# Optimization experiments

Measured on AMD Instinct MI355X. Metric: run time of the kernel, lower is better.

The kernel has to match this reference:

```python
import jax, jax.numpy as jnp
import numpy as np

N = 1024      # nodes == subgraphs (NGNN: one subgraph per node)
DEG = 8       # average degree
E = N * DEG   # edges
IND = 32      # indim
OUTD = 32     # outdim


def setup_inputs() -> dict:
    key = jax.random.key(0)
    k0, k1, k2, k3, k4 = jax.random.split(key, 5)
    X = jax.random.normal(k0, (N, N, IND), dtype=jnp.float32)
    # binary tuple-support mask (which (i,j) tuples exist in the sparse 2D tensor)
    mask = jax.random.randint(k1, (N, N), 0, 2).astype(jnp.int32)
    # adjacency edge list: A[row, col] = 1 (structure-only sparse adjacency)
    edge_row = jax.random.randint(k2, (E,), 0, N)  # destination j
    edge_col = jax.random.randint(k3, (E,), 0, N)  # source k
    # MLP (single linear layer, PygHO MLP default)
    W = jax.random.normal(k4, (IND, OUTD), dtype=jnp.float32) / np.sqrt(IND).astype(np.float32)
    b = jnp.zeros((OUTD,), dtype=jnp.float32)
    return {"X": X, "mask": mask, "edge_row": edge_row, "edge_col": edge_col, "W": W, "b": b}


def reference(X, mask, edge_row, edge_col, W, b):
    n = X.shape[0]
    m = mask.astype(X.dtype)[..., None]                      # [n, n, 1]
    # tuplewise MLP on existing tuples: tX[i,j] = X[i,j] @ W + b
    tX = (jnp.einsum("ijd,de->ije", X, W) + b) * m           # [n, n, OUTD]
    # message passing within each subgraph i along node dim j:
    # ret[i, j] = sum_{k : A[j,k]=1} tX[i, k]
    msgs = jnp.take(tX, edge_col, axis=1)                    # [n, E, OUTD] gather sources
    msgs = jnp.moveaxis(msgs, 1, 0)                          # [E, n, OUTD]
    agg = jax.ops.segment_sum(msgs, edge_row, num_segments=n)  # [j, i, OUTD]
    ret = jnp.swapaxes(agg, 0, 1) * m                        # restrict to tuple support (tarX = tX)
    return ret
```

## Files before the change

### kernel.cpp

```cpp
#include <hip/hip_runtime.h>


#define NN   1024
#define IND  32
#define OUTD 32
#define EE   8192

typedef __attribute__((ext_vector_type(2))) float f32x2;

__global__ __launch_bounds__(1024) void k_zero(int* __restrict__ p, int n) {
    const int t = blockIdx.x * 1024 + threadIdx.x;
    if (t < n) p[t] = 0;
}

__global__ __launch_bounds__(1024) void k_count(const int* __restrict__ erow,
                                                int* __restrict__ cnt, int n_edges) {
    const int e = blockIdx.x * 1024 + threadIdx.x;
    if (e < n_edges) atomicAdd(&cnt[erow[e]], 1);
}

__global__ __launch_bounds__(1024) void k_scan(const int* __restrict__ cnt,
                                               int* __restrict__ row_ptr,
                                               int* __restrict__ fill) {
    __shared__ int sb[NN];
    const int t = threadIdx.x;
    const int v = cnt[t];
    sb[t] = v;
    __syncthreads();
    #pragma unroll
    for (int off = 1; off < NN; off <<= 1) {
        const int a = (t >= off) ? sb[t - off] : 0;
        __syncthreads();
        sb[t] += a;
        __syncthreads();
    }
    const int excl = sb[t] - v;
    row_ptr[t] = excl;
    fill[t]    = excl;
    if (t == NN - 1) row_ptr[NN] = sb[t];
}

__global__ __launch_bounds__(1024) void k_scatter(const int* __restrict__ erow,
                                                  const int* __restrict__ ecol,
                                                  int* __restrict__ fill,
                                                  int* __restrict__ cols, int n_edges) {
    const int e = blockIdx.x * 1024 + threadIdx.x;
    if (e < n_edges) {
        const int pos = atomicAdd(&fill[erow[e]], 1);
        cols[pos] = ecol[e];
    }
}

__global__ __launch_bounds__(256, 4) void ngnn_main_kernel(
    const float* __restrict__ X, const int* __restrict__ mask,
    const float* __restrict__ W, const float* __restrict__ b,
    const int* __restrict__ row_ptr, const int* __restrict__ cols,
    float* __restrict__ out)
{
    __shared__ float          maskf[NN];
    __shared__ unsigned int   meta[NN];
    __shared__ unsigned short colsl[EE];
    __shared__ unsigned short alist[NN];
    __shared__ int            acount;

    const int t = threadIdx.x;
    const int i = blockIdx.x;

    if (t == 0) acount = 0;
    {
        const int4 m4 = ((const int4*)(mask + (size_t)i * NN))[t];
        maskf[4*t+0] = (float)m4.x; maskf[4*t+1] = (float)m4.y;
        maskf[4*t+2] = (float)m4.z; maskf[4*t+3] = (float)m4.w;
    }
    __syncthreads();

    #pragma unroll
    for (int p = 0; p < 4; ++p) {
        const int j = p * 256 + t;
        if (maskf[j] != 0.f) {
            const int a   = row_ptr[j];
            const int bnd = row_ptr[j + 1];
            int c = 0;
            for (int e = a; e < bnd; ++e) {
                const int k = cols[e] & (NN - 1);
                if (maskf[k] != 0.f) colsl[a + (c++)] = (unsigned short)k;
            }
            meta[j] = (unsigned)a | ((unsigned)c << 16);
            const int pos = atomicAdd(&acount, 1);
            alist[pos] = (unsigned short)j;
        }
    }
    __syncthreads();

    const float4 z = {0.f, 0.f, 0.f, 0.f};
    #pragma unroll
    for (int p = 0; p < 4; ++p) {
        const int j = p * 256 + t;
        if (maskf[j] == 0.f) {
            float4* orow = (float4*)(out + ((size_t)i * NN + j) * OUTD);
            #pragma unroll
            for (int q = 0; q < 8; ++q) orow[q] = z;
        }
    }

    const float4* Xi = (const float4*)(X + (size_t)i * NN * IND);
    const f32x2*  W2 = (const f32x2*)W;
    const f32x2*  b2 = (const f32x2*)b;
    const int na = acount;

    for (int a = t; a < na; a += 256) {
        const int j = (int)alist[a];
        const unsigned md = meta[j];
        const int e0 = (int)(md & 0xffffu);
        const int cn = (int)(md >> 16);

        float4 S4[8];
        #pragma unroll
        for (int s = 0; s < 8; ++s) S4[s] = z;

        for (int q = 0; q < cn; ++q) {
            const int k = (int)colsl[e0 + q];
            const float4* r = Xi + (k << 3);
            #pragma unroll
            for (int s = 0; s < 8; ++s) {
                const float4 v = r[s];
                S4[s].x += v.x; S4[s].y += v.y; S4[s].z += v.z; S4[s].w += v.w;
            }
        }

        const float cf = (float)cn;
        f32x2 o2[16];
        #pragma unroll
        for (int c = 0; c < 16; ++c) o2[c] = b2[c] * cf;
        #pragma unroll
        for (int d = 0; d < IND; ++d) {
            const float sd = ((const float*)S4)[d];
            #pragma unroll
            for (int c = 0; c < 16; ++c) o2[c] += W2[d * 16 + c] * sd;
        }

        float4* orow = (float4*)(out + ((size_t)i * NN + j) * OUTD);
        #pragma unroll
        for (int q2 = 0; q2 < 8; ++q2)
            orow[q2] = make_float4(o2[2*q2].x, o2[2*q2].y, o2[2*q2+1].x, o2[2*q2+1].y);
    }
}

extern "C" void kernel_launch(void* const* d_in, const int* in_sizes, int n_in,
                              void* d_out, int out_size, void* d_ws, size_t ws_size,
                              hipStream_t stream) {
    const float* X    = (const float*)d_in[0];
    const int*   mask = (const int*)d_in[1];
    const int*   erow = (const int*)d_in[2];
    const int*   ecol = (const int*)d_in[3];
    const float* W    = (const float*)d_in[4];
    const float* b    = (const float*)d_in[5];
    float*       out  = (float*)d_out;

    int n_edges = in_sizes[2];
    if (n_edges > EE) n_edges = EE;

    int* cnt     = (int*)d_ws;
    int* row_ptr = cnt + 1024;
    int* fill    = cnt + 2560;
    int* cols    = cnt + 4096;

    const int eb = (n_edges + 1023) / 1024;
    k_zero   <<<1, 1024, 0, stream>>>(cnt, NN);
    k_count  <<<eb, 1024, 0, stream>>>(erow, cnt, n_edges);
    k_scan   <<<1, 1024, 0, stream>>>(cnt, row_ptr, fill);
    k_scatter<<<eb, 1024, 0, stream>>>(erow, ecol, fill, cols, n_edges);

    ngnn_main_kernel<<<NN, 256, 0, stream>>>(X, mask, W, b, row_ptr, cols, out);
}
```

Baseline: 335.9 us.

## Fuse CSR build into one kernel and map output channels to lanes

Combines the four CSR-building kernels into a single-block kernel that counts, scans and scatters in shared memory, which removes launch overhead. The main kernel is restructured so that each wavefront handles two rows, with each lane owning one channel. Lanes gather X coalesced per channel, share partial sums through LDS, and do the 32x32 linear layer from W values held in registers. This replaces the old per-thread, row-serial gather and its big register arrays with coalesced accesses and less register pressure, at the cost of per-row LDS exchange and scalar stores.

```diff
diff --git a/kernel.cpp b/kernel.cpp
--- a/kernel.cpp
+++ b/kernel.cpp
@@ -6,28 +6,29 @@
 #define OUTD 32
 #define EE   8192
 
-typedef __attribute__((ext_vector_type(2))) float f32x2;
+__global__ __launch_bounds__(1024) void k_csr(const int* __restrict__ erow,
+                                              const int* __restrict__ ecol,
+                                              int* __restrict__ row_ptr,
+                                              int* __restrict__ cols,
+                                              int n_edges) {
+    __shared__ int sb[NN];
+    __shared__ int fill[NN];
+    const int t = threadIdx.x;
 
-__global__ __launch_bounds__(1024) void k_zero(int* __restrict__ p, int n) {
-    const int t = blockIdx.x * 1024 + threadIdx.x;
-    if (t < n) p[t] = 0;
-}
-
-__global__ __launch_bounds__(1024) void k_count(const int* __restrict__ erow,
-                                                int* __restrict__ cnt, int n_edges) {
-    const int e = blockIdx.x * 1024 + threadIdx.x;
-    if (e < n_edges) atomicAdd(&cnt[erow[e]], 1);
-}
-
-__global__ __launch_bounds__(1024) void k_scan(const int* __restrict__ cnt,
-                                               int* __restrict__ row_ptr,
-                                               int* __restrict__ fill) {
-    __shared__ int sb[NN];
-    const int t = threadIdx.x;
-    const int v = cnt[t];
-    sb[t] = v;
+    int er[8], ec[8];
+    #pragma unroll
+    for (int it = 0; it < 8; ++it) {
+        const int e = it * 1024 + t;
+        er[it] = (e < n_edges) ? (erow[e] & (NN - 1)) : -1;
+        ec[it] = (e < n_edges) ? (ecol[e] & (NN - 1)) : 0;
+    }
+    sb[t] = 0;
     __syncthreads();
     #pragma unroll
+    for (int it = 0; it < 8; ++it)
+        if (er[it] >= 0) atomicAdd(&sb[er[it]], 1);
+    __syncthreads();
+    const int v = sb[t];
     for (int off = 1; off < NN; off <<= 1) {
         const int a = (t >= off) ? sb[t - off] : 0;
         __syncthreads();
@@ -38,17 +39,13 @@
     row_ptr[t] = excl;
     fill[t]    = excl;
     if (t == NN - 1) row_ptr[NN] = sb[t];
-}
-
-__global__ __launch_bounds__(1024) void k_scatter(const int* __restrict__ erow,
-                                                  const int* __restrict__ ecol,
-                                                  int* __restrict__ fill,
-                                                  int* __restrict__ cols, int n_edges) {
-    const int e = blockIdx.x * 1024 + threadIdx.x;
-    if (e < n_edges) {
-        const int pos = atomicAdd(&fill[erow[e]], 1);
-        cols[pos] = ecol[e];
-    }
+    __syncthreads();
+    #pragma unroll
+    for (int it = 0; it < 8; ++it)
+        if (er[it] >= 0) {
+            const int pos = atomicAdd(&fill[er[it]], 1);
+            cols[pos] = ec[it];
+        }
 }
 
 __global__ __launch_bounds__(256, 4) void ngnn_main_kernel(
@@ -61,10 +58,20 @@
     __shared__ unsigned int   meta[NN];
     __shared__ unsigned short colsl[EE];
     __shared__ unsigned short alist[NN];
+    __shared__ float          Sbuf[4][64];
     __shared__ int            acount;
 
     const int t = threadIdx.x;
     const int i = blockIdx.x;
+    const int l = t & 63;
+    const int w = t >> 6;
+    const int h = l >> 5;
+    const int d = l & 31;
+
+    float wl[IND];
+    #pragma unroll
+    for (int dd = 0; dd < IND; ++dd) wl[dd] = W[dd * OUTD + d];
+    const float b_c = b[d];
 
     if (t == 0) acount = 0;
     {
@@ -103,46 +110,51 @@
         }
     }
 
-    const float4* Xi = (const float4*)(X + (size_t)i * NN * IND);
-    const f32x2*  W2 = (const f32x2*)W;
-    const f32x2*  b2 = (const f32x2*)b;
+    const float* Xd = X + (size_t)i * NN * IND + d;
     const int na = acount;
 
-    for (int a = t; a < na; a += 256) {
-        const int j = (int)alist[a];
-        const unsigned md = meta[j];
+    for (int p = w; 2 * p < na; p += 4) {
+        const int idx  = 2 * p + h;
+        const int live = (idx < na) ? 1 : 0;
+        const int j    = live ? (int)alist[idx] : 0;
+        const unsigned md = live ? meta[j] : 0u;
         const int e0 = (int)(md & 0xffffu);
         const int cn = (int)(md >> 16);
 
-        float4 S4[8];
-        #pragma unroll
-        for (int s = 0; s < 8; ++s) S4[s] = z;
+        float S = 0.f;
+        int q = 0;
+        for (; q + 4 <= cn; q += 4) {
+            const int k0 = (int)colsl[e0 + q + 0];
+            const int k1 = (int)colsl[e0 + q + 1];
+            const int k2 = (int)colsl[e0 + q + 2];
+            const int k3 = (int)colsl[e0 + q + 3];
+            const float v0 = Xd[(size_t)k0 << 5];
+            const float v1 = Xd[(size_t)k1 << 5];
+            const float v2 = Xd[(size_t)k2 << 5];
+            const float v3 = Xd[(size_t)k3 << 5];
+            S += (v0 + v1) + (v2 + v3);
+        }
+        for (; q < cn; ++q)
+            S += Xd[(size_t)colsl[e0 + q] << 5];
 
-        for (int q = 0; q < cn; ++q) {
-            const int k = (int)colsl[e0 + q];
-            const float4* r = Xi + (k << 3);
-            #pragma unroll
-            for (int s = 0; s < 8; ++s) {
-                const float4 v = r[s];
-                S4[s].x += v.x; S4[s].y += v.y; S4[s].z += v.z; S4[s].w += v.w;
-            }
-        }
+        Sbuf[w][l] = S;
+        asm volatile("s_waitcnt lgkmcnt(0)" ::: "memory");
 
         const float cf = (float)cn;
-        f32x2 o2[16];
+        const float4* Sb = (const float4*)&Sbuf[w][h << 5];
+        float o0 = b_c * cf, o1 = 0.f, o2 = 0.f, o3 = 0.f;
         #pragma unroll
-        for (int c = 0; c < 16; ++c) o2[c] = b2[c] * cf;
-        #pragma unroll
-        for (int d = 0; d < IND; ++d) {
-            const float sd = ((const float*)S4)[d];
-            #pragma unroll
-            for (int c = 0; c < 16; ++c) o2[c] += W2[d * 16 + c] * sd;
+        for (int qq = 0; qq < 8; ++qq) {
+            const float4 s4 = Sb[qq];
+            o0 = fmaf(s4.x, wl[4*qq+0], o0);
+            o1 = fmaf(s4.y, wl[4*qq+1], o1);
+            o2 = fmaf(s4.z, wl[4*qq+2], o2);
+            o3 = fmaf(s4.w, wl[4*qq+3], o3);
         }
+        const float o = (o0 + o1) + (o2 + o3);
 
-        float4* orow = (float4*)(out + ((size_t)i * NN + j) * OUTD);
-        #pragma unroll
-        for (int q2 = 0; q2 < 8; ++q2)
-            orow[q2] = make_float4(o2[2*q2].x, o2[2*q2].y, o2[2*q2+1].x, o2[2*q2+1].y);
+        if (live)
+            out[((size_t)i * NN + j) * OUTD + d] = o;
     }
 }
 
@@ -160,16 +172,9 @@
     int n_edges = in_sizes[2];
     if (n_edges > EE) n_edges = EE;
 
-    int* cnt     = (int*)d_ws;
-    int* row_ptr = cnt + 1024;
-    int* fill    = cnt + 2560;
-    int* cols    = cnt + 4096;
+    int* row_ptr = (int*)d_ws;
+    int* cols    = row_ptr + 2048;
 
-    const int eb = (n_edges + 1023) / 1024;
-    k_zero   <<<1, 1024, 0, stream>>>(cnt, NN);
-    k_count  <<<eb, 1024, 0, stream>>>(erow, cnt, n_edges);
-    k_scan   <<<1, 1024, 0, stream>>>(cnt, row_ptr, fill);
-    k_scatter<<<eb, 1024, 0, stream>>>(erow, ecol, fill, cols, n_edges);
-
+    k_csr<<<1, 1024, 0, stream>>>(erow, ecol, row_ptr, cols, n_edges);
     ngnn_main_kernel<<<NN, 256, 0, stream>>>(X, mask, W, b, row_ptr, cols, out);
 }
```

Result: slower. 377.2 us (+12.3%).
